# Performance work log

Measured on AMD Instinct MI355X. Metric: run time of the kernel, lower is better.

## Reference

```python
import jax, jax.numpy as jnp
import numpy as np

B, S, D, H = 4, 2048, 1024, 16
DK = D // H

def setup_inputs() -> dict:
    key = jax.random.key(0)
    ks = jax.random.split(key, 11)
    scale = 1.0 / np.sqrt(D)
    return {
        "query": jax.random.normal(ks[0], (B, S, D), jnp.float32),
        "key_": jax.random.normal(ks[1], (B, S, D), jnp.float32),
        "value": jax.random.normal(ks[2], (B, S, D), jnp.float32),
        "Wq": jax.random.normal(ks[3], (D, D), jnp.float32) * scale,
        "bq": jnp.zeros((D,), jnp.float32),
        "Wk": jax.random.normal(ks[4], (D, D), jnp.float32) * scale,
        "bk": jnp.zeros((D,), jnp.float32),
        "Wv": jax.random.normal(ks[5], (D, D), jnp.float32) * scale,
        "bv": jnp.zeros((D,), jnp.float32),
        "Wo": jax.random.normal(ks[6], (D, D), jnp.float32) * scale,
        "bo": jnp.zeros((D,), jnp.float32),
    }

def reference(query, key_, value, Wq, bq, Wk, bk, Wv, bv, Wo, bo):
    # Linear projections (torch Linear: x @ W.T + b)
    Q = query @ Wq.T + bq            # [B,S,D]
    K = key_ @ Wk.T + bk
    V = value @ Wv.T + bv
    # split heads -> [B,H,S,DK]
    def split(x):
        return x.reshape(B, S, H, DK).transpose(0, 2, 1, 3)
    Qh, Kh, Vh = split(Q), split(K), split(V)
    scores = jnp.einsum("bhqd,bhkd->bhqk", Qh, Kh) / np.sqrt(DK)
    attn = jax.nn.softmax(scores, axis=-1)
    ctx = jnp.einsum("bhqk,bhkd->bhqd", attn, Vh)
    ctx = ctx.transpose(0, 2, 1, 3).reshape(B, S, D)
    return ctx @ Wo.T + bo
```

## Files before the change

### kernel.cpp

```cpp
#include <hip/hip_runtime.h>
#include <hip/hip_bf16.h>
#include <stdint.h>

#define B_ 4
#define S_ 2048
#define D_ 1024
#define H_ 16
#define DK_ 64
#define GM (B_ * S_)
#define GN D_
#define GK D_
#define BM 128
#define BN 128
#define BK 64
#define QBLK 128

typedef __attribute__((ext_vector_type(8))) __bf16 bf16x8;
typedef __attribute__((ext_vector_type(4))) float f32x4;
typedef __attribute__((ext_vector_type(4))) uint32_t u32x4;
typedef __attribute__((ext_vector_type(2))) uint32_t u32x2;

#if __has_builtin(__builtin_amdgcn_exp2f)
#define EXP2F(x) __builtin_amdgcn_exp2f(x)
#else
#define EXP2F(x) exp2f(x)
#endif

#define SCALE_LOG2E 0.18033688011112042f

__device__ __forceinline__ uint16_t f2bf(float x) {
  uint32_t u = __builtin_bit_cast(uint32_t, x);
  u += 0x7fffu + ((u >> 16) & 1u);
  return (uint16_t)(u >> 16);
}
__device__ __forceinline__ uint32_t cvtpk(float lo, float hi) {
  uint32_t r;
  asm("v_cvt_pk_bf16_f32 %0, %1, %2" : "=v"(r) : "v"(lo), "v"(hi));
  return r;
}
__device__ __forceinline__ void gload_lds16(const void* g, void* l) {
  __builtin_amdgcn_global_load_lds(
      (const __attribute__((address_space(1))) void*)g,
      (__attribute__((address_space(3))) void*)l, 16, 0, 0);
}

struct CvtArgs {
  const float* src[7];
  uint16_t* dst[7];
  int n[7];
  float scale[7];
};

__global__ __launch_bounds__(256) void cvt_f32_bf16(CvtArgs a) {
  const int z = blockIdx.z;
  const float* __restrict__ s = a.src[z];
  uint16_t* __restrict__ d = a.dst[z];
  const float sc = a.scale[z];
  const int nv = a.n[z] >> 3;
  const int stride = gridDim.x * blockDim.x;
  for (int i = blockIdx.x * blockDim.x + threadIdx.x; i < nv; i += stride) {
    f32x4 v0 = *(const f32x4*)(s + (size_t)i * 8);
    f32x4 v1 = *(const f32x4*)(s + (size_t)i * 8 + 4);
    union { uint16_t u[8]; u32x4 q; } o;
#pragma unroll
    for (int j = 0; j < 4; ++j) o.u[j] = f2bf(v0[j] * sc);
#pragma unroll
    for (int j = 0; j < 4; ++j) o.u[4 + j] = f2bf(v1[j] * sc);
    *(u32x4*)(d + (size_t)i * 8) = o.q;
  }
}

struct Gemm3Args {
  const uint16_t* A[3];
  const uint16_t* W[3];
  const float* bias[3];
  float bscale[3];
  void* C[3];
};

template <bool CF32>
__global__ __launch_bounds__(256, 2) void mha_gemm3(Gemm3Args args) {
  const int z = blockIdx.z;
  const char* __restrict__ A = (const char*)args.A[z];
  const char* __restrict__ W = (const char*)args.W[z];
  const float* __restrict__ bias = args.bias[z];
  const float bsc = args.bscale[z];
  void* __restrict__ C = args.C[z];

  __shared__ alignas(16) uint16_t tA[BM][BK];
  __shared__ alignas(16) uint16_t tW[BN][BK];

  const int tid = threadIdx.x;
  const int lane = tid & 63;
  const int wid = tid >> 6;
  const int wm = wid >> 1, wn = wid & 1;
  const int l16 = lane & 15, g = lane >> 4;

  const int m0 = blockIdx.y * BM;
  const int n0 = blockIdx.x * BN;

  f32x4 acc[4][4] = {};
  const int o = tid * 16;

  for (int k0 = 0; k0 < GK; k0 += BK) {
#pragma unroll
    for (int i = 0; i < 4; ++i) {
      const int oo = o + i * 4096;
      const int row = oo >> 7, colb = oo & 127;
      gload_lds16(A + (size_t)(m0 + row) * (GK * 2) + (size_t)k0 * 2 + colb,
                  ((char*)&tA[0][0]) + i * 4096 + wid * 1024);
      gload_lds16(W + (size_t)(n0 + row) * (GK * 2) + (size_t)k0 * 2 + colb,
                  ((char*)&tW[0][0]) + i * 4096 + wid * 1024);
    }
    __syncthreads();
#pragma unroll
    for (int kk = 0; kk < 2; ++kk) {
      const int kcol = kk * 32 + g * 8;
      bf16x8 af[4], bfr[4];
#pragma unroll
      for (int m = 0; m < 4; ++m)
        af[m] = *(const bf16x8*)&tA[wm * 64 + m * 16 + l16][kcol];
#pragma unroll
      for (int n = 0; n < 4; ++n)
        bfr[n] = *(const bf16x8*)&tW[wn * 64 + n * 16 + l16][kcol];
#pragma unroll
      for (int m = 0; m < 4; ++m)
#pragma unroll
        for (int n = 0; n < 4; ++n)
          acc[m][n] = __builtin_amdgcn_mfma_f32_16x16x32_bf16(
              af[m], bfr[n], acc[m][n], 0, 0, 0);
    }
    __syncthreads();
  }

#pragma unroll
  for (int n = 0; n < 4; ++n) {
    const int col = n0 + wn * 64 + n * 16 + l16;
    const float bv = bias[col] * bsc;
#pragma unroll
    for (int m = 0; m < 4; ++m) {
      const int rbase = m0 + wm * 64 + m * 16 + g * 4;
#pragma unroll
      for (int r = 0; r < 4; ++r) {
        const float v = acc[m][n][r] + bv;
        if (CF32)
          ((float*)C)[(size_t)(rbase + r) * GN + col] = v;
        else
          ((uint16_t*)C)[(size_t)(rbase + r) * GN + col] = f2bf(v);
      }
    }
  }
}

__global__ __launch_bounds__(256) void transpose_v(
    const uint16_t* __restrict__ Vp, uint16_t* __restrict__ Vt) {
  __shared__ alignas(16) char T[64 * 128];
  const int tid = threadIdx.x;
  const int s0 = blockIdx.x * 64;
  const int h = blockIdx.y;
  const int bb = blockIdx.z;
#pragma unroll
  for (int it = 0; it < 2; ++it) {
    const int idx = tid + it * 256;
    const int row = idx >> 3;
    const int colb = (idx & 7) * 16;
    const u32x4 v = *(const u32x4*)((const char*)Vp +
        (((size_t)bb * S_ + s0 + row) * D_ + h * DK_) * 2 + colb);
    *(u32x4*)(T + row * 128 + (colb ^ (((row >> 3) & 7) << 4))) = v;
  }
  __syncthreads();
#pragma unroll
  for (int it = 0; it < 2; ++it) {
    const int idx = tid + it * 256;
    const int dk = idx >> 3;
    const int sc = (idx & 7) * 8;
    union { uint16_t u[8]; u32x4 q; } o;
#pragma unroll
    for (int j = 0; j < 8; ++j) {
      const int row = sc + j;
      o.u[j] =
          *(const uint16_t*)(T + row * 128 + ((dk * 2) ^ (((row >> 3) & 7) << 4)));
    }
    *(u32x4*)((char*)Vt +
              (((size_t)(bb * H_ + h) * DK_ + dk) * S_ + s0 + sc) * 2) = o.q;
  }
}

__global__ __launch_bounds__(256) void mha_attn(
    const uint16_t* __restrict__ Q, const uint16_t* __restrict__ K,
    const uint16_t* __restrict__ Vt, uint16_t* __restrict__ O) {
  __shared__ alignas(16) char K_s[2][8192];
  __shared__ alignas(16) char V_s[2][8192];

  const int tid = threadIdx.x;
  const int lane = tid & 63;
  const int wid = tid >> 6;
  const int l16 = lane & 15, g = lane >> 4;
  const int bh = blockIdx.y;
  const int b = bh >> 4, h = bh & 15;
  const int q0 = blockIdx.x * QBLK;

  bf16x8 qf[2][2];
#pragma unroll
  for (int mi = 0; mi < 2; ++mi) {
    const uint16_t* qp = Q + ((size_t)(b * S_) + q0 + mi * 64 + wid * 16 + l16) * D_ +
                         h * DK_ + g * 8;
    qf[mi][0] = *(const bf16x8*)qp;
    qf[mi][1] = *(const bf16x8*)(qp + 32);
  }

  f32x4 o_acc[2][4] = {};
  float lpart[2] = {0.f, 0.f};

  const char* Kb = (const char*)K;
  const char* Vtb = (const char*)Vt;

  int srow[2], scol[2];
#pragma unroll
  for (int i = 0; i < 2; ++i) {
    const int oo = tid * 16 + i * 4096;
    srow[i] = oo >> 7;
    scol[i] = (oo & 127) ^ ((srow[i] & 7) << 4);
  }

#define ISSUE_LOADS(buf, kv0)                                                  \
  {                                                                            \
    _Pragma("unroll") for (int i = 0; i < 2; ++i) {                            \
      gload_lds16(Kb + (((size_t)b * S_ + (kv0) + srow[i]) * D_ + h * DK_) * 2 \
                      + scol[i],                                               \
                  &K_s[buf][0] + i * 4096 + wid * 1024);                       \
      gload_lds16(Vtb + (((size_t)bh * DK_ + srow[i]) * S_ + (kv0)) * 2        \
                      + scol[i],                                               \
                  &V_s[buf][0] + i * 4096 + wid * 1024);                       \
    }                                                                          \
  }

  ISSUE_LOADS(0, 0);
  __syncthreads();
  int cur = 0;

  const int bsrc = l16 + ((g & 1) << 5);
  const int gsel = g >> 1;

  for (int kv0 = 0; kv0 < S_; kv0 += 64) {
    const bool last = (kv0 + 64 >= S_);
    if (!last) ISSUE_LOADS(cur ^ 1, kv0 + 64);

    f32x4 sacc[2][4] = {};
#pragma unroll
    for (int ks = 0; ks < 2; ++ks) {
      const int kcolb = ks * 64 + g * 16;
#pragma unroll
      for (int n = 0; n < 4; ++n) {
        const int kvr = n * 16 + l16;
        const bf16x8 kf =
            *(const bf16x8*)(&K_s[cur][0] + kvr * 128 + (kcolb ^ ((kvr & 7) << 4)));
#pragma unroll
        for (int mi = 0; mi < 2; ++mi)
          sacc[mi][n] = __builtin_amdgcn_mfma_f32_16x16x32_bf16(
              kf, qf[mi][ks], sacc[mi][n], 0, 0, 0);
      }
    }

    uint32_t pb[2][2][4];
#pragma unroll
    for (int mi = 0; mi < 2; ++mi) {
      uint32_t pk0[4][2];
#pragma unroll
      for (int n = 0; n < 4; ++n) {
        float e0 = EXP2F(sacc[mi][n][0]);
        float e1 = EXP2F(sacc[mi][n][1]);
        float e2 = EXP2F(sacc[mi][n][2]);
        float e3 = EXP2F(sacc[mi][n][3]);
        lpart[mi] += (e0 + e1) + (e2 + e3);
        pk0[n][0] = cvtpk(e0, e1);
        pk0[n][1] = cvtpk(e2, e3);
      }
#pragma unroll
      for (int ks = 0; ks < 2; ++ks)
#pragma unroll
        for (int jp = 0; jp < 4; ++jp) {
          const int srcl = bsrc + ((jp >> 1) << 4);
          const uint32_t va = __shfl(pk0[2 * ks][jp & 1], srcl, 64);
          const uint32_t vb = __shfl(pk0[2 * ks + 1][jp & 1], srcl, 64);
          pb[mi][ks][jp] = gsel ? vb : va;
        }
    }

#pragma unroll
    for (int ks = 0; ks < 2; ++ks) {
      const int kcolb = ks * 64 + g * 16;
      bf16x8 pf[2];
#pragma unroll
      for (int mi = 0; mi < 2; ++mi) {
        u32x4 t = {pb[mi][ks][0], pb[mi][ks][1], pb[mi][ks][2], pb[mi][ks][3]};
        pf[mi] = __builtin_bit_cast(bf16x8, t);
      }
#pragma unroll
      for (int n = 0; n < 4; ++n) {
        const int dkr = n * 16 + l16;
        const bf16x8 vf =
            *(const bf16x8*)(&V_s[cur][0] + dkr * 128 + (kcolb ^ ((dkr & 7) << 4)));
#pragma unroll
        for (int mi = 0; mi < 2; ++mi)
          o_acc[mi][n] = __builtin_amdgcn_mfma_f32_16x16x32_bf16(
              vf, pf[mi], o_acc[mi][n], 0, 0, 0);
      }
    }

    if (!last) __syncthreads();
    cur ^= 1;
  }

  float linv[2];
#pragma unroll
  for (int mi = 0; mi < 2; ++mi) {
    float s_ = lpart[mi];
    s_ += __shfl_xor(s_, 16, 64);
    s_ += __shfl_xor(s_, 32, 64);
    linv[mi] = 1.f / s_;
  }
#pragma unroll
  for (int mi = 0; mi < 2; ++mi) {
    const size_t row = (size_t)b * S_ + q0 + mi * 64 + wid * 16 + l16;
    uint16_t* op = O + row * D_ + h * DK_ + g * 4;
#pragma unroll
    for (int n = 0; n < 4; ++n) {
      u32x2 w;
      w[0] = cvtpk(o_acc[mi][n][0] * linv[mi], o_acc[mi][n][1] * linv[mi]);
      w[1] = cvtpk(o_acc[mi][n][2] * linv[mi], o_acc[mi][n][3] * linv[mi]);
      *(u32x2*)(op + n * 16) = w;
    }
  }
}

extern "C" void kernel_launch(void* const* d_in, const int* in_sizes, int n_in,
                              void* d_out, int out_size, void* d_ws,
                              size_t ws_size, hipStream_t stream) {
  (void)in_sizes; (void)n_in; (void)out_size; (void)ws_size;

  const float* query = (const float*)d_in[0];
  const float* key_ = (const float*)d_in[1];
  const float* value = (const float*)d_in[2];
  const float* Wq = (const float*)d_in[3];
  const float* bq = (const float*)d_in[4];
  const float* Wk = (const float*)d_in[5];
  const float* bk = (const float*)d_in[6];
  const float* Wv = (const float*)d_in[7];
  const float* bv = (const float*)d_in[8];
  const float* Wo = (const float*)d_in[9];
  const float* bo = (const float*)d_in[10];

  const size_t nact = (size_t)GM * GN;
  const size_t nw = (size_t)GN * GK;
  uint16_t* p = (uint16_t*)d_ws;
  uint16_t* qb = p; p += nact;
  uint16_t* kb = p; p += nact;
  uint16_t* vb = p; p += nact;
  uint16_t* wq = p; p += nw;
  uint16_t* wk = p; p += nw;
  uint16_t* wv = p; p += nw;
  uint16_t* wo = p; p += nw;
  uint16_t* Qp = p; p += nact;
  uint16_t* Kp = p; p += nact;
  uint16_t* Vp = p; p += nact;
  uint16_t* Cp = p; p += nact;
  uint16_t* Vt = qb;

  CvtArgs ca;
  const float* srcs[7] = {query, key_, value, Wq, Wk, Wv, Wo};
  uint16_t* dsts[7] = {qb, kb, vb, wq, wk, wv, wo};
  const int cnts[7] = {(int)nact, (int)nact, (int)nact, (int)nw,
                       (int)nw,   (int)nw,   (int)nw};
  for (int i = 0; i < 7; ++i) {
    ca.src[i] = srcs[i]; ca.dst[i] = dsts[i]; ca.n[i] = cnts[i];
    ca.scale[i] = 1.0f;
  }
  ca.scale[3] = SCALE_LOG2E;
  cvt_f32_bf16<<<dim3(512, 1, 7), dim3(256), 0, stream>>>(ca);

  Gemm3Args g1;
  g1.A[0] = qb; g1.A[1] = kb; g1.A[2] = vb;
  g1.W[0] = wq; g1.W[1] = wk; g1.W[2] = wv;
  g1.bias[0] = bq; g1.bias[1] = bk; g1.bias[2] = bv;
  g1.bscale[0] = SCALE_LOG2E; g1.bscale[1] = 1.0f; g1.bscale[2] = 1.0f;
  g1.C[0] = Qp; g1.C[1] = Kp; g1.C[2] = Vp;
  mha_gemm3<false>
      <<<dim3(GN / BN, GM / BM, 3), dim3(256), 0, stream>>>(g1);

  transpose_v<<<dim3(S_ / 64, H_, B_), dim3(256), 0, stream>>>(Vp, Vt);

  mha_attn<<<dim3(S_ / QBLK, B_ * H_), dim3(256), 0, stream>>>(Qp, Kp, Vt, Cp);

  Gemm3Args g2;
  g2.A[0] = Cp; g2.W[0] = wo; g2.bias[0] = bo; g2.C[0] = d_out;
  g2.bscale[0] = 1.0f;
  g2.A[1] = g2.A[0]; g2.W[1] = g2.W[0]; g2.bias[1] = g2.bias[0]; g2.C[1] = g2.C[0];
  g2.bscale[1] = 1.0f;
  g2.A[2] = g2.A[0]; g2.W[2] = g2.W[0]; g2.bias[2] = g2.bias[0]; g2.C[2] = g2.C[0];
  g2.bscale[2] = 1.0f;
  mha_gemm3<true>
      <<<dim3(GN / BN, GM / BM, 1), dim3(256), 0, stream>>>(g2);
}
```

Baseline: 267.7 us.

## Double KV tile to 128 in attention and remap grid for head locality

Raises the KV block processed per iteration from 64 to 128 rows, doubling the LDS buffers and per-iteration MFMA work so that there are half as many barriers and loop iterations. Also flattens the launch grid to 1D and remaps block indices so that groups of 8 consecutive blocks cover different heads of the same query tile, aiming to improve L2 locality across the blocks that run together. In exchange it uses 64KB of LDS and more registers per thread (sacc and pk0 double), which can lower occupancy.

```diff
diff --git a/kernel.cpp b/kernel.cpp
--- a/kernel.cpp
+++ b/kernel.cpp
@@ -14,6 +14,7 @@
 #define BN 128
 #define BK 64
 #define QBLK 128
+#define KVBLK 128
 
 typedef __attribute__((ext_vector_type(8))) __bf16 bf16x8;
 typedef __attribute__((ext_vector_type(4))) float f32x4;
@@ -189,16 +190,19 @@
 __global__ __launch_bounds__(256) void mha_attn(
     const uint16_t* __restrict__ Q, const uint16_t* __restrict__ K,
     const uint16_t* __restrict__ Vt, uint16_t* __restrict__ O) {
-  __shared__ alignas(16) char K_s[2][8192];
-  __shared__ alignas(16) char V_s[2][8192];
+  __shared__ alignas(16) char K_s[2][16384];
+  __shared__ alignas(16) char V_s[2][16384];
 
   const int tid = threadIdx.x;
   const int lane = tid & 63;
   const int wid = tid >> 6;
   const int l16 = lane & 15, g = lane >> 4;
-  const int bh = blockIdx.y;
+
+  const int d = blockIdx.x;
+  const int bh = (d & 7) + ((d >> 7) << 3);
+  const int qb = (d >> 3) & 15;
   const int b = bh >> 4, h = bh & 15;
-  const int q0 = blockIdx.x * QBLK;
+  const int q0 = qb * QBLK;
 
   bf16x8 qf[2][2];
 #pragma unroll
@@ -215,22 +219,24 @@
   const char* Kb = (const char*)K;
   const char* Vtb = (const char*)Vt;
 
-  int srow[2], scol[2];
-#pragma unroll
-  for (int i = 0; i < 2; ++i) {
+  int srowK[4], scolK[4], srowV[4], scolV[4];
+#pragma unroll
+  for (int i = 0; i < 4; ++i) {
     const int oo = tid * 16 + i * 4096;
-    srow[i] = oo >> 7;
-    scol[i] = (oo & 127) ^ ((srow[i] & 7) << 4);
+    srowK[i] = oo >> 7;
+    scolK[i] = (oo & 127) ^ ((srowK[i] & 7) << 4);
+    srowV[i] = oo >> 8;
+    scolV[i] = (oo & 255) ^ ((srowV[i] & 7) << 4);
   }
 
 #define ISSUE_LOADS(buf, kv0)                                                  \
   {                                                                            \
-    _Pragma("unroll") for (int i = 0; i < 2; ++i) {                            \
-      gload_lds16(Kb + (((size_t)b * S_ + (kv0) + srow[i]) * D_ + h * DK_) * 2 \
-                      + scol[i],                                               \
+    _Pragma("unroll") for (int i = 0; i < 4; ++i) {                            \
+      gload_lds16(Kb + (((size_t)b * S_ + (kv0) + srowK[i]) * D_ + h * DK_) * 2\
+                      + scolK[i],                                              \
                   &K_s[buf][0] + i * 4096 + wid * 1024);                       \
-      gload_lds16(Vtb + (((size_t)bh * DK_ + srow[i]) * S_ + (kv0)) * 2        \
-                      + scol[i],                                               \
+      gload_lds16(Vtb + (((size_t)bh * DK_ + srowV[i]) * S_ + (kv0)) * 2       \
+                      + scolV[i],                                              \
                   &V_s[buf][0] + i * 4096 + wid * 1024);                       \
     }                                                                          \
   }
@@ -242,16 +248,16 @@
   const int bsrc = l16 + ((g & 1) << 5);
   const int gsel = g >> 1;
 
-  for (int kv0 = 0; kv0 < S_; kv0 += 64) {
-    const bool last = (kv0 + 64 >= S_);
-    if (!last) ISSUE_LOADS(cur ^ 1, kv0 + 64);
-
-    f32x4 sacc[2][4] = {};
+  for (int kv0 = 0; kv0 < S_; kv0 += KVBLK) {
+    const bool last = (kv0 + KVBLK >= S_);
+    if (!last) ISSUE_LOADS(cur ^ 1, kv0 + KVBLK);
+
+    f32x4 sacc[2][8] = {};
 #pragma unroll
     for (int ks = 0; ks < 2; ++ks) {
       const int kcolb = ks * 64 + g * 16;
 #pragma unroll
-      for (int n = 0; n < 4; ++n) {
+      for (int n = 0; n < 8; ++n) {
         const int kvr = n * 16 + l16;
         const bf16x8 kf =
             *(const bf16x8*)(&K_s[cur][0] + kvr * 128 + (kcolb ^ ((kvr & 7) << 4)));
@@ -262,12 +268,12 @@
       }
     }
 
-    uint32_t pb[2][2][4];
+    uint32_t pb[2][4][4];
 #pragma unroll
     for (int mi = 0; mi < 2; ++mi) {
-      uint32_t pk0[4][2];
-#pragma unroll
-      for (int n = 0; n < 4; ++n) {
+      uint32_t pk0[8][2];
+#pragma unroll
+      for (int n = 0; n < 8; ++n) {
         float e0 = EXP2F(sacc[mi][n][0]);
         float e1 = EXP2F(sacc[mi][n][1]);
         float e2 = EXP2F(sacc[mi][n][2]);
@@ -277,7 +283,7 @@
         pk0[n][1] = cvtpk(e2, e3);
       }
 #pragma unroll
-      for (int ks = 0; ks < 2; ++ks)
+      for (int ks = 0; ks < 4; ++ks)
 #pragma unroll
         for (int jp = 0; jp < 4; ++jp) {
           const int srcl = bsrc + ((jp >> 1) << 4);
@@ -288,7 +294,7 @@
     }
 
 #pragma unroll
-    for (int ks = 0; ks < 2; ++ks) {
+    for (int ks = 0; ks < 4; ++ks) {
       const int kcolb = ks * 64 + g * 16;
       bf16x8 pf[2];
 #pragma unroll
@@ -300,7 +306,7 @@
       for (int n = 0; n < 4; ++n) {
         const int dkr = n * 16 + l16;
         const bf16x8 vf =
-            *(const bf16x8*)(&V_s[cur][0] + dkr * 128 + (kcolb ^ ((dkr & 7) << 4)));
+            *(const bf16x8*)(&V_s[cur][0] + dkr * 256 + (kcolb ^ ((dkr & 7) << 4)));
 #pragma unroll
         for (int mi = 0; mi < 2; ++mi)
           o_acc[mi][n] = __builtin_amdgcn_mfma_f32_16x16x32_bf16(
@@ -390,7 +396,7 @@
 
   transpose_v<<<dim3(S_ / 64, H_, B_), dim3(256), 0, stream>>>(Vp, Vt);
 
-  mha_attn<<<dim3(S_ / QBLK, B_ * H_), dim3(256), 0, stream>>>(Qp, Kp, Vt, Cp);
+  mha_attn<<<dim3((S_ / QBLK) * B_ * H_), dim3(256), 0, stream>>>(Qp, Kp, Vt, Cp);
 
   Gemm3Args g2;
   g2.A[0] = Cp; g2.W[0] = wo; g2.bias[0] = bo; g2.C[0] = d_out;
```

Measured after the change: 253.0 us (median of 3 runs). 5.5% less time.
